# Kernel optimization log

Hardware: AMD Instinct MI355X
Metric: run time of the kernel (lower is better)

## Reference

```python
import jax, jax.numpy as jnp
import numpy as np

D_MODEL = 768
N_HEADS = 12
D_K = D_MODEL // N_HEADS
NEG = -1e9


def setup_inputs() -> dict:
    key = jax.random.key(0)
    ks = jax.random.split(key, 10)
    B, S = 2, 2048
    x = jax.random.normal(ks[0], (B, S, D_MODEL), dtype=jnp.float32)
    # causal mask, broadcastable over batch and heads
    mask = jnp.tril(jnp.ones((S, S), dtype=jnp.int32))[None, None]
    scale = 1.0 / np.sqrt(D_MODEL)
    def lin(k):
        return jax.random.normal(k, (D_MODEL, D_MODEL), dtype=jnp.float32) * scale
    return {
        "x": x, "mask": mask,
        "wq": lin(ks[1]), "bq": jnp.zeros((D_MODEL,), jnp.float32),
        "wk": lin(ks[2]), "bk": jnp.zeros((D_MODEL,), jnp.float32),
        "wv": lin(ks[3]), "bv": jnp.zeros((D_MODEL,), jnp.float32),
        "wo": lin(ks[4]), "bo": jnp.zeros((D_MODEL,), jnp.float32),
    }


def reference(x, mask, wq, bq, wk, bk, wv, bv, wo, bo):
    B, S, _ = x.shape
    def split_heads(t):  # [B,S,D] -> [B,H,S,dk]
        return t.reshape(B, S, N_HEADS, D_K).transpose(0, 2, 1, 3)
    q = split_heads(x @ wq + bq)
    k = split_heads(x @ wk + bk)
    v = split_heads(x @ wv + bv)
    scores = jnp.einsum("bhqd,bhkd->bhqk", q, k) / jnp.sqrt(jnp.float32(D_K))
    scores = jnp.where(mask == 0, NEG, scores)
    attn = jax.nn.softmax(scores, axis=-1)
    # dropout is identity in eval mode
    ctx = jnp.einsum("bhqk,bhkd->bhqd", attn, v)
    ctx = ctx.transpose(0, 2, 1, 3).reshape(B, S, D_MODEL)
    return ctx @ wo + bo
```

## Files before the change

kernel.cpp:

```cpp
#include <hip/hip_runtime.h>
#include <hip/hip_bf16.h>
#include <stdint.h>

#define DM   768
#define NH   12
#define DKH  64
#define BB   2
#define SS   2048
#define MT   (BB*SS)
#define NQKV (3*DM)

typedef __attribute__((ext_vector_type(8))) short short8;
typedef __attribute__((ext_vector_type(4))) float f32x4;

__device__ __forceinline__ unsigned short f2bf(float f) {
    union { float f; unsigned u; } v; v.f = f;
    unsigned r = v.u + 0x7fffu + ((v.u >> 16) & 1u);
    return (unsigned short)(r >> 16);
}

__device__ __forceinline__ void gload_lds16(const unsigned short* g, unsigned short* l) {
    __builtin_amdgcn_global_load_lds((const __attribute__((address_space(1))) void*)g,
                                     (__attribute__((address_space(3))) void*)l, 16, 0, 0);
}

__launch_bounds__(256)
__global__ void k_conv(const float* __restrict__ x, unsigned short* __restrict__ xb,
                       const float* __restrict__ wq, const float* __restrict__ wk,
                       const float* __restrict__ wv, const float* __restrict__ wo,
                       unsigned short* __restrict__ wT) {
    __shared__ float tile[32][33];
    const int t = threadIdx.x;
    if (blockIdx.x < 3072) {
        int i = blockIdx.x * 256 + t;
        const float4 v = ((const float4*)x)[i];
        ushort4 o;
        o.x = f2bf(v.x); o.y = f2bf(v.y); o.z = f2bf(v.z); o.w = f2bf(v.w);
        ((ushort4*)xb)[i] = o;
    } else {
        const int cid = blockIdx.x - 3072;
        const int sel = cid / 576;
        const int rem = cid - sel * 576;
        const int kb = rem / 24, nb = rem - (rem / 24) * 24;
        const float* w = (sel == 0) ? wq : (sel == 1) ? wk : (sel == 2) ? wv : wo;
        const int k0 = kb * 32, n0 = nb * 32;
        const int tx = t & 31, ty = t >> 5;
        #pragma unroll
        for (int j = 0; j < 4; j++)
            tile[ty + 8*j][tx] = w[(size_t)(k0 + ty + 8*j) * DM + n0 + tx];
        __syncthreads();
        #pragma unroll
        for (int j = 0; j < 4; j++)
            wT[(size_t)(sel*DM + n0 + ty + 8*j) * DM + k0 + tx] = f2bf(tile[tx][ty + 8*j]);
    }
}

__launch_bounds__(256, 4)
__global__ void k_gemm_qkv(const unsigned short* __restrict__ xb,
                           const unsigned short* __restrict__ wT,
                           const float* __restrict__ bq, const float* __restrict__ bk,
                           const float* __restrict__ bv,
                           unsigned short* __restrict__ Qb,
                           unsigned short* __restrict__ Kb,
                           unsigned short* __restrict__ Vt) {
    __shared__ __align__(16) unsigned short As[128*64];
    __shared__ __align__(16) unsigned short Bs[64*64];
    const int t = threadIdx.x;
    const int m0 = blockIdx.x * 128;
    const int n0 = blockIdx.y * 64;
    const int wid = t >> 6, lane = t & 63, q4 = lane >> 4, l16 = lane & 15;
    const int wm = (wid >> 1) * 64, wn = (wid & 1) * 32;

    const int srow = lane >> 3;
    const int scol = ((lane & 7) ^ srow) * 8;
    const unsigned short* Ag = xb + (size_t)(m0 + wid*8 + srow) * DM + scol;
    const unsigned short* Bg = wT + (size_t)(n0 + wid*8 + srow) * DM + scol;
    unsigned short* ldsA = &As[(wid*8)*64];
    unsigned short* ldsB = &Bs[(wid*8)*64];
    const int swz = (l16 & 7) * 8;

    f32x4 acc[4][2];
    for (int i = 0; i < 4; i++) for (int j = 0; j < 2; j++)
        acc[i][j] = (f32x4){0.f, 0.f, 0.f, 0.f};

    for (int kt = 0; kt < DM; kt += 64) {
        #pragma unroll
        for (int j = 0; j < 4; j++)
            gload_lds16(Ag + (size_t)(j*32) * DM + kt, ldsA + j*32*64);
        #pragma unroll
        for (int j = 0; j < 2; j++)
            gload_lds16(Bg + (size_t)(j*32) * DM + kt, ldsB + j*32*64);
        __syncthreads();
        #pragma unroll
        for (int kc = 0; kc < 2; kc++) {
            short8 af[4], bf[2];
            #pragma unroll
            for (int i = 0; i < 4; i++)
                af[i] = *(const short8*)&As[(wm + i*16 + l16)*64 + ((kc*32 + q4*8) ^ swz)];
            #pragma unroll
            for (int i = 0; i < 2; i++)
                bf[i] = *(const short8*)&Bs[(wn + i*16 + l16)*64 + ((kc*32 + q4*8) ^ swz)];
            #pragma unroll
            for (int mi = 0; mi < 4; mi++)
                #pragma unroll
                for (int ni = 0; ni < 2; ni++)
                    acc[mi][ni] = __builtin_amdgcn_mfma_f32_16x16x32_bf16(af[mi], bf[ni], acc[mi][ni], 0, 0, 0);
        }
        __syncthreads();
    }

    const int sel = n0 / DM;
    const float* bias = (sel == 0) ? bq : (sel == 1) ? bk : bv;
    for (int ni = 0; ni < 2; ni++) {
        const int col = n0 + wn + ni*16 + l16;
        const int c = col - sel * DM;
        const float bsv = bias[c];
        const int h = c >> 6, d = c & 63;
        for (int mi = 0; mi < 4; mi++) {
            for (int r = 0; r < 4; r++) {
                const int row = m0 + wm + mi*16 + q4*4 + r;
                const int b = row >> 11, s = row & 2047;
                const int bh = b * NH + h;
                float v = acc[mi][ni][r] + bsv;
                if (sel == 0) {
                    Qb[(bh*SS + s)*DKH + d] = f2bf(v * 0.125f);
                } else if (sel == 1) {
                    Kb[(bh*SS + s)*DKH + d] = f2bf(v);
                } else {
                    Vt[(bh*DKH + d)*SS + s] = f2bf(v);
                }
            }
        }
    }
}

__device__ const int UNITS[48] = {
  (15<<16)|(0<<8)|16, (31<<16)|(0<<8)|16, (31<<16)|(16<<8)|32, (30<<16)|(0<<8)|16,
  (14<<16)|(0<<8)|15, (29<<16)|(0<<8)|15, (29<<16)|(15<<8)|30, (28<<16)|(0<<8)|15, (30<<16)|(16<<8)|31,
  (13<<16)|(0<<8)|14, (27<<16)|(0<<8)|14, (27<<16)|(14<<8)|28, (26<<16)|(0<<8)|14, (28<<16)|(15<<8)|29,
  (12<<16)|(0<<8)|13, (25<<16)|(0<<8)|13, (25<<16)|(13<<8)|26, (24<<16)|(0<<8)|13, (26<<16)|(14<<8)|27,
  (11<<16)|(0<<8)|12, (23<<16)|(0<<8)|12, (23<<16)|(12<<8)|24, (22<<16)|(0<<8)|12, (24<<16)|(13<<8)|25,
  (10<<16)|(0<<8)|11, (21<<16)|(0<<8)|11, (21<<16)|(11<<8)|22, (20<<16)|(0<<8)|11, (22<<16)|(12<<8)|23,
  ( 9<<16)|(0<<8)|10, (19<<16)|(0<<8)|10, (19<<16)|(10<<8)|20, (18<<16)|(0<<8)|10, (20<<16)|(11<<8)|21,
  ( 8<<16)|(0<<8)| 9, (17<<16)|(0<<8)| 9, (17<<16)|( 9<<8)|18, (16<<16)|(0<<8)| 9, (18<<16)|(10<<8)|19,
  ( 7<<16)|(0<<8)| 8, (16<<16)|( 9<<8)|17,
  ( 6<<16)|(0<<8)| 7, ( 5<<16)|(0<<8)| 6, ( 4<<16)|(0<<8)| 5, ( 3<<16)|(0<<8)| 4,
  ( 2<<16)|(0<<8)| 3, ( 1<<16)|(0<<8)| 2, ( 0<<16)|(0<<8)| 1,
};

__launch_bounds__(256, 4)
__global__ void k_attn(const unsigned short* __restrict__ Qb,
                       const unsigned short* __restrict__ Kb,
                       const unsigned short* __restrict__ Vt,
                       unsigned short* __restrict__ ctx,
                       float* __restrict__ Opart, float* __restrict__ lpart) {
    __shared__ __align__(16) unsigned short Ks[2][64*64];
    __shared__ __align__(16) unsigned short Vs[2][64*64];
    __shared__ __align__(16) unsigned short P2[4][16*64];
    const int t = threadIdx.x;
    const int wid = t >> 6, lane = t & 63, q4 = lane >> 4, l16 = lane & 15;

    const int lin = blockIdx.x;
    const int bh = lin % 24;
    const int info = UNITS[lin / 24];
    const int qblk = info >> 16, t0 = (info >> 8) & 0xff, t1 = info & 0xff;
    const int b = bh / NH, h = bh - b * NH;
    const int qw = qblk * 64 + wid * 16;

    const unsigned short* Qp = Qb + (size_t)bh * SS * DKH;
    const unsigned short* Kp = Kb + (size_t)bh * SS * DKH;
    const unsigned short* Vp = Vt + (size_t)bh * DKH * SS;

    const int sr  = t >> 3;
    const int sc8 = (t & 7) * 8;
    const int scs = sc8 ^ ((sr & 7) * 8);
    const int swz = (l16 & 7) * 8;

    short8 qf[2];
    qf[0] = *(const short8*)(Qp + (size_t)(qw + l16)*DKH +      q4*8);
    qf[1] = *(const short8*)(Qp + (size_t)(qw + l16)*DKH + 32 + q4*8);

    f32x4 accO[4];
    #pragma unroll
    for (int j = 0; j < 4; j++) accO[j] = (f32x4){0.f, 0.f, 0.f, 0.f};
    float lacc = 0.f;

    {
        const int kb0 = t0 * 64;
        *(uint4*)&Ks[0][ sr    *64 + scs] = *(const uint4*)(Kp + (size_t)(kb0 + sr)     *DKH + sc8);
        *(uint4*)&Ks[0][(sr+32)*64 + scs] = *(const uint4*)(Kp + (size_t)(kb0 + sr + 32)*DKH + sc8);
        *(uint4*)&Vs[0][ sr    *64 + scs] = *(const uint4*)(Vp + (size_t) sr     *SS + kb0 + sc8);
        *(uint4*)&Vs[0][(sr+32)*64 + scs] = *(const uint4*)(Vp + (size_t)(sr+32) *SS + kb0 + sc8);
    }
    __syncthreads();

    for (int kt = t0; kt < t1; kt++) {
        const int cb = (kt - t0) & 1, nb = cb ^ 1;
        const bool hasN = (kt + 1 < t1);
        uint4 nk0, nk1, nv0, nv1;
        if (hasN) {
            const int kn = (kt + 1) * 64;
            nk0 = *(const uint4*)(Kp + (size_t)(kn + sr)      * DKH + sc8);
            nk1 = *(const uint4*)(Kp + (size_t)(kn + sr + 32) * DKH + sc8);
            nv0 = *(const uint4*)(Vp + (size_t)(sr)      * SS + kn + sc8);
            nv1 = *(const uint4*)(Vp + (size_t)(sr + 32) * SS + kn + sc8);
        }
        f32x4 St[4];
        #pragma unroll
        for (int ni = 0; ni < 4; ni++) St[ni] = (f32x4){0.f, 0.f, 0.f, 0.f};
        __builtin_amdgcn_s_setprio(1);
        #pragma unroll
        for (int ni = 0; ni < 4; ni++) {
            const int rbase = (ni*16 + l16) * 64;
            short8 kf0 = *(const short8*)&Ks[cb][rbase + ((     q4*8) ^ swz)];
            short8 kf1 = *(const short8*)&Ks[cb][rbase + ((32 + q4*8) ^ swz)];
            St[ni] = __builtin_amdgcn_mfma_f32_16x16x32_bf16(kf0, qf[0], St[ni], 0, 0, 0);
            St[ni] = __builtin_amdgcn_mfma_f32_16x16x32_bf16(kf1, qf[1], St[ni], 0, 0, 0);
        }
        __builtin_amdgcn_s_setprio(0);
        if (kt < qblk) {
            #pragma unroll
            for (int ni = 0; ni < 4; ni++) {
                float p0 = __expf(St[ni][0]), p1 = __expf(St[ni][1]);
                float p2 = __expf(St[ni][2]), p3 = __expf(St[ni][3]);
                lacc += (p0 + p1) + (p2 + p3);
                union { __hip_bfloat162 v; unsigned u; } u01, u23;
                u01.v = __float22bfloat162_rn(make_float2(p0, p1));
                u23.v = __float22bfloat162_rn(make_float2(p2, p3));
                uint2 pk; pk.x = u01.u; pk.y = u23.u;
                *(uint2*)&P2[wid][l16*64 + ((ni*16 + q4*4) ^ swz)] = pk;
            }
        } else {
            const int qrow = qw + l16;
            #pragma unroll
            for (int ni = 0; ni < 4; ni++) {
                const int key0 = kt*64 + ni*16 + q4*4;
                float p[4];
                #pragma unroll
                for (int r = 0; r < 4; r++) {
                    p[r] = (key0 + r > qrow) ? 0.f : __expf(St[ni][r]);
                    lacc += p[r];
                }
                union { __hip_bfloat162 v; unsigned u; } u01, u23;
                u01.v = __float22bfloat162_rn(make_float2(p[0], p[1]));
                u23.v = __float22bfloat162_rn(make_float2(p[2], p[3]));
                uint2 pk; pk.x = u01.u; pk.y = u23.u;
                *(uint2*)&P2[wid][l16*64 + ((ni*16 + q4*4) ^ swz)] = pk;
            }
        }
        asm volatile("s_waitcnt lgkmcnt(0)" ::: "memory");
        short8 pf[2];
        pf[0] = *(const short8*)&P2[wid][l16*64 + ((     q4*8) ^ swz)];
        pf[1] = *(const short8*)&P2[wid][l16*64 + ((32 + q4*8) ^ swz)];
        __builtin_amdgcn_s_setprio(1);
        #pragma unroll
        for (int ndi = 0; ndi < 4; ndi++) {
            const int rbase = (ndi*16 + l16) * 64;
            short8 vf0 = *(const short8*)&Vs[cb][rbase + ((     q4*8) ^ swz)];
            short8 vf1 = *(const short8*)&Vs[cb][rbase + ((32 + q4*8) ^ swz)];
            accO[ndi] = __builtin_amdgcn_mfma_f32_16x16x32_bf16(vf0, pf[0], accO[ndi], 0, 0, 0);
            accO[ndi] = __builtin_amdgcn_mfma_f32_16x16x32_bf16(vf1, pf[1], accO[ndi], 0, 0, 0);
        }
        __builtin_amdgcn_s_setprio(0);
        if (hasN) {
            *(uint4*)&Ks[nb][ sr    *64 + scs] = nk0;
            *(uint4*)&Ks[nb][(sr+32)*64 + scs] = nk1;
            *(uint4*)&Vs[nb][ sr    *64 + scs] = nv0;
            *(uint4*)&Vs[nb][(sr+32)*64 + scs] = nv1;
        }
        __syncthreads();
    }

    float l = lacc;
    l += __shfl_xor(l, 16);
    l += __shfl_xor(l, 32);

    if (qblk < 16) {
        const float inv = 1.0f / l;
        const size_t row = (size_t)(b*SS + qw + l16);
        #pragma unroll
        for (int ndi = 0; ndi < 4; ndi++) {
            ushort4 o;
            o.x = f2bf(accO[ndi][0] * inv);
            o.y = f2bf(accO[ndi][1] * inv);
            o.z = f2bf(accO[ndi][2] * inv);
            o.w = f2bf(accO[ndi][3] * inv);
            *(ushort4*)&ctx[row*DM + h*64 + ndi*16 + q4*4] = o;
        }
    } else {
        const int pair  = bh * 16 + (qblk - 16);
        const int chunk = (t0 != 0);
        const int qloc  = wid * 16 + l16;
        float* Op = Opart + ((size_t)pair * 2 + chunk) * 4096;
        #pragma unroll
        for (int ndi = 0; ndi < 4; ndi++)
            *(f32x4*)&Op[qloc*64 + ndi*16 + q4*4] = accO[ndi];
        if (q4 == 0) lpart[pair*128 + chunk*64 + qloc] = l;
    }
}

__launch_bounds__(256)
__global__ void k_combine(const float* __restrict__ Opart,
                          const float* __restrict__ lpart,
                          unsigned short* __restrict__ ctx) {
    const int pair = blockIdx.x;
    const int bh = pair >> 4, qblk = 16 + (pair & 15);
    const int b = bh / NH, h = bh - b * NH;
    const int t = threadIdx.x;
    const int q = t >> 2, dg = (t & 3) * 16;
    const float* P0 = Opart + (size_t)pair * 2 * 4096;
    const float* P1 = P0 + 4096;
    const float* L0 = lpart + pair * 128;
    const float inv = 1.0f / (L0[q] + L0[64 + q]);
    const size_t row = (size_t)(b*SS + qblk*64 + q);
    #pragma unroll
    for (int i = 0; i < 4; i++) {
        f32x4 a = *(const f32x4*)&P0[q*64 + dg + i*4];
        f32x4 c = *(const f32x4*)&P1[q*64 + dg + i*4];
        ushort4 o;
        o.x = f2bf((a[0] + c[0]) * inv);
        o.y = f2bf((a[1] + c[1]) * inv);
        o.z = f2bf((a[2] + c[2]) * inv);
        o.w = f2bf((a[3] + c[3]) * inv);
        *(ushort4*)&ctx[row*DM + h*64 + dg + i*4] = o;
    }
}

__launch_bounds__(256)
__global__ void k_gemm_proj(const unsigned short* __restrict__ ctx,
                            const unsigned short* __restrict__ woT,
                            const float* __restrict__ bo,
                            float* __restrict__ out) {
    __shared__ __align__(16) unsigned short As[128][32];
    __shared__ __align__(16) unsigned short Bs[64][32];
    const int t = threadIdx.x;
    const int m0 = blockIdx.x * 128;
    const int n0 = blockIdx.y * 64;
    const int wid = t >> 6, lane = t & 63, q4 = lane >> 4, l16 = lane & 15;
    const int wm = (wid >> 1) * 64, wn = (wid & 1) * 32;

    const int srowA = wid * 32 + (lane >> 2);
    const int srowB = wid * 16 + (lane >> 2);
    const int koff = (lane & 3) * 8;
    const unsigned short* AgL = ctx + (size_t)(m0 + srowA) * DM + koff;
    const unsigned short* AgH = AgL + (size_t)16 * DM;
    const unsigned short* BgL = woT + (size_t)(n0 + srowB) * DM + koff;
    unsigned short* ldsA1 = &As[wid*32][0];
    unsigned short* ldsA2 = &As[wid*32 + 16][0];
    unsigned short* ldsB1 = &Bs[wid*16][0];

    f32x4 acc[4][2];
    for (int i = 0; i < 4; i++) for (int j = 0; j < 2; j++)
        acc[i][j] = (f32x4){0.f, 0.f, 0.f, 0.f};

    for (int kt = 0; kt < DM; kt += 32) {
        gload_lds16(AgL + kt, ldsA1);
        gload_lds16(AgH + kt, ldsA2);
        gload_lds16(BgL + kt, ldsB1);
        __syncthreads();
        short8 af[4], bf[2];
        for (int i = 0; i < 4; i++) af[i] = *(const short8*)&As[wm + i*16 + l16][q4*8];
        for (int i = 0; i < 2; i++) bf[i] = *(const short8*)&Bs[wn + i*16 + l16][q4*8];
        for (int mi = 0; mi < 4; mi++)
            for (int ni = 0; ni < 2; ni++)
                acc[mi][ni] = __builtin_amdgcn_mfma_f32_16x16x32_bf16(af[mi], bf[ni], acc[mi][ni], 0, 0, 0);
        __syncthreads();
    }

    for (int ni = 0; ni < 2; ni++) {
        const int col = n0 + wn + ni*16 + l16;
        const float bsv = bo[col];
        for (int mi = 0; mi < 4; mi++) {
            for (int r = 0; r < 4; r++) {
                const int row = m0 + wm + mi*16 + q4*4 + r;
                out[(size_t)row * DM + col] = acc[mi][ni][r] + bsv;
            }
        }
    }
}

extern "C" void kernel_launch(void* const* d_in, const int* in_sizes, int n_in,
                              void* d_out, int out_size, void* d_ws, size_t ws_size,
                              hipStream_t stream) {
    const float* x  = (const float*)d_in[0];
    const float* wq = (const float*)d_in[2];
    const float* bq = (const float*)d_in[3];
    const float* wk = (const float*)d_in[4];
    const float* bk = (const float*)d_in[5];
    const float* wv = (const float*)d_in[6];
    const float* bv = (const float*)d_in[7];
    const float* wo = (const float*)d_in[8];
    const float* bo = (const float*)d_in[9];
    float* out = (float*)d_out;

    unsigned short* xb  = (unsigned short*)d_ws;
    unsigned short* wT  = xb + (size_t)MT * DM;
    unsigned short* Qb  = wT + (size_t)4 * DM * DM;
    unsigned short* Kb  = Qb + (size_t)BB * NH * SS * DKH;
    unsigned short* Vt  = Kb + (size_t)BB * NH * SS * DKH;
    unsigned short* ctx = Vt + (size_t)BB * NH * SS * DKH;
    float* Opart = (float*)(ctx + (size_t)MT * DM);
    float* lpart = Opart + (size_t)768 * 4096;

    k_conv<<<3072 + 2304, 256, 0, stream>>>(x, xb, wq, wk, wv, wo, wT);
    dim3 g1(MT / 128, NQKV / 64);
    k_gemm_qkv<<<g1, 256, 0, stream>>>(xb, wT, bq, bk, bv, Qb, Kb, Vt);
    k_attn<<<dim3(1152), 256, 0, stream>>>(Qb, Kb, Vt, ctx, Opart, lpart);
    k_combine<<<dim3(384), 256, 0, stream>>>(Opart, lpart, ctx);
    dim3 g3(MT / 128, DM / 64);
    k_gemm_proj<<<g3, 256, 0, stream>>>(ctx, wT + (size_t)3 * DM * DM, bo, out);
}
```

Before: 170.7 us.

## Stage V transpose through LDS and retile output projection to 64x64 swizzled tiles

In the QKV GEMM epilogue, V blocks now write their bf16 tile into shared memory with an XOR swizzle, then store transposed rows to Vt with 16-byte vector stores. The old path did strided 2-byte scattered stores. The output projection GEMM moves from 128x64 tiles with a K-step of 32 to 64x64 tiles with a K-step of 64 and swizzled LDS, doubling the grid and adding occupancy hints. This is meant to improve memory coalescing and occupancy, at the cost of an extra barrier in the epilogue and less reuse per tile in the projection.

```diff
diff --git a/kernel.cpp b/kernel.cpp
--- a/kernel.cpp
+++ b/kernel.cpp
@@ -110,26 +110,50 @@
     }
 
     const int sel = n0 / DM;
-    const float* bias = (sel == 0) ? bq : (sel == 1) ? bk : bv;
-    for (int ni = 0; ni < 2; ni++) {
-        const int col = n0 + wn + ni*16 + l16;
-        const int c = col - sel * DM;
-        const float bsv = bias[c];
-        const int h = c >> 6, d = c & 63;
-        for (int mi = 0; mi < 4; mi++) {
-            for (int r = 0; r < 4; r++) {
-                const int row = m0 + wm + mi*16 + q4*4 + r;
-                const int b = row >> 11, s = row & 2047;
-                const int bh = b * NH + h;
-                float v = acc[mi][ni][r] + bsv;
-                if (sel == 0) {
-                    Qb[(bh*SS + s)*DKH + d] = f2bf(v * 0.125f);
-                } else if (sel == 1) {
-                    Kb[(bh*SS + s)*DKH + d] = f2bf(v);
-                } else {
-                    Vt[(bh*DKH + d)*SS + s] = f2bf(v);
+    if (sel < 2) {
+        const float* bias = (sel == 0) ? bq : bk;
+        for (int ni = 0; ni < 2; ni++) {
+            const int col = n0 + wn + ni*16 + l16;
+            const int c = col - sel * DM;
+            const float bsv = bias[c];
+            const int h = c >> 6, d = c & 63;
+            for (int mi = 0; mi < 4; mi++) {
+                for (int r = 0; r < 4; r++) {
+                    const int row = m0 + wm + mi*16 + q4*4 + r;
+                    const int b = row >> 11, s = row & 2047;
+                    const int bh = b * NH + h;
+                    float v = acc[mi][ni][r] + bsv;
+                    if (sel == 0) Qb[(bh*SS + s)*DKH + d] = f2bf(v * 0.125f);
+                    else          Kb[(bh*SS + s)*DKH + d] = f2bf(v);
                 }
             }
+        }
+    } else {
+        const int h  = (n0 - 2*DM) >> 6;
+        const int bb = m0 >> 11, sbase = m0 & 2047;
+        const int bh = bb * NH + h;
+        #pragma unroll
+        for (int ni = 0; ni < 2; ni++) {
+            const int c = wn + ni*16 + l16;
+            const float bsv = bv[h*64 + c];
+            #pragma unroll
+            for (int mi = 0; mi < 4; mi++) {
+                const int rowb = wm + mi*16 + q4*4;
+                ushort4 o;
+                o.x = f2bf(acc[mi][ni][0] + bsv);
+                o.y = f2bf(acc[mi][ni][1] + bsv);
+                o.z = f2bf(acc[mi][ni][2] + bsv);
+                o.w = f2bf(acc[mi][ni][3] + bsv);
+                *(ushort4*)&As[c*128 + (rowb ^ ((c & 7) * 8))] = o;
+            }
+        }
+        __syncthreads();
+        const int d = t >> 2, sq = (t & 3) * 32;
+        unsigned short* Vg = Vt + ((size_t)bh*DKH + d)*SS + sbase + sq;
+        #pragma unroll
+        for (int j = 0; j < 4; j++) {
+            short8 v = *(const short8*)&As[d*128 + ((sq + j*8) ^ ((d & 7) * 8))];
+            *(short8*)&Vg[j*8] = v;
         }
     }
 }
@@ -326,51 +350,60 @@
     }
 }
 
-__launch_bounds__(256)
+__launch_bounds__(256, 4)
 __global__ void k_gemm_proj(const unsigned short* __restrict__ ctx,
                             const unsigned short* __restrict__ woT,
                             const float* __restrict__ bo,
                             float* __restrict__ out) {
-    __shared__ __align__(16) unsigned short As[128][32];
-    __shared__ __align__(16) unsigned short Bs[64][32];
+    __shared__ __align__(16) unsigned short As[64*64];
+    __shared__ __align__(16) unsigned short Bs[64*64];
     const int t = threadIdx.x;
-    const int m0 = blockIdx.x * 128;
+    const int m0 = blockIdx.x * 64;
     const int n0 = blockIdx.y * 64;
     const int wid = t >> 6, lane = t & 63, q4 = lane >> 4, l16 = lane & 15;
-    const int wm = (wid >> 1) * 64, wn = (wid & 1) * 32;
-
-    const int srowA = wid * 32 + (lane >> 2);
-    const int srowB = wid * 16 + (lane >> 2);
-    const int koff = (lane & 3) * 8;
-    const unsigned short* AgL = ctx + (size_t)(m0 + srowA) * DM + koff;
-    const unsigned short* AgH = AgL + (size_t)16 * DM;
-    const unsigned short* BgL = woT + (size_t)(n0 + srowB) * DM + koff;
-    unsigned short* ldsA1 = &As[wid*32][0];
-    unsigned short* ldsA2 = &As[wid*32 + 16][0];
-    unsigned short* ldsB1 = &Bs[wid*16][0];
-
-    f32x4 acc[4][2];
-    for (int i = 0; i < 4; i++) for (int j = 0; j < 2; j++)
+    const int wm = (wid >> 1) * 32, wn = (wid & 1) * 32;
+
+    const int srow = lane >> 3;
+    const int scol = ((lane & 7) ^ srow) * 8;
+    const unsigned short* Ag = ctx + (size_t)(m0 + wid*8 + srow) * DM + scol;
+    const unsigned short* Bg = woT + (size_t)(n0 + wid*8 + srow) * DM + scol;
+    unsigned short* ldsA = &As[(wid*8)*64];
+    unsigned short* ldsB = &Bs[(wid*8)*64];
+    const int swz = (l16 & 7) * 8;
+
+    f32x4 acc[2][2];
+    for (int i = 0; i < 2; i++) for (int j = 0; j < 2; j++)
         acc[i][j] = (f32x4){0.f, 0.f, 0.f, 0.f};
 
-    for (int kt = 0; kt < DM; kt += 32) {
-        gload_lds16(AgL + kt, ldsA1);
-        gload_lds16(AgH + kt, ldsA2);
-        gload_lds16(BgL + kt, ldsB1);
-        __syncthreads();
-        short8 af[4], bf[2];
-        for (int i = 0; i < 4; i++) af[i] = *(const short8*)&As[wm + i*16 + l16][q4*8];
-        for (int i = 0; i < 2; i++) bf[i] = *(const short8*)&Bs[wn + i*16 + l16][q4*8];
-        for (int mi = 0; mi < 4; mi++)
-            for (int ni = 0; ni < 2; ni++)
-                acc[mi][ni] = __builtin_amdgcn_mfma_f32_16x16x32_bf16(af[mi], bf[ni], acc[mi][ni], 0, 0, 0);
+    for (int kt = 0; kt < DM; kt += 64) {
+        #pragma unroll
+        for (int j = 0; j < 2; j++) {
+            gload_lds16(Ag + (size_t)(j*32) * DM + kt, ldsA + j*32*64);
+            gload_lds16(Bg + (size_t)(j*32) * DM + kt, ldsB + j*32*64);
+        }
+        __syncthreads();
+        #pragma unroll
+        for (int kc = 0; kc < 2; kc++) {
+            short8 af[2], bf[2];
+            #pragma unroll
+            for (int i = 0; i < 2; i++)
+                af[i] = *(const short8*)&As[(wm + i*16 + l16)*64 + ((kc*32 + q4*8) ^ swz)];
+            #pragma unroll
+            for (int i = 0; i < 2; i++)
+                bf[i] = *(const short8*)&Bs[(wn + i*16 + l16)*64 + ((kc*32 + q4*8) ^ swz)];
+            #pragma unroll
+            for (int mi = 0; mi < 2; mi++)
+                #pragma unroll
+                for (int ni = 0; ni < 2; ni++)
+                    acc[mi][ni] = __builtin_amdgcn_mfma_f32_16x16x32_bf16(af[mi], bf[ni], acc[mi][ni], 0, 0, 0);
+        }
         __syncthreads();
     }
 
     for (int ni = 0; ni < 2; ni++) {
         const int col = n0 + wn + ni*16 + l16;
         const float bsv = bo[col];
-        for (int mi = 0; mi < 4; mi++) {
+        for (int mi = 0; mi < 2; mi++) {
             for (int r = 0; r < 4; r++) {
                 const int row = m0 + wm + mi*16 + q4*4 + r;
                 out[(size_t)row * DM + col] = acc[mi][ni][r] + bsv;
@@ -407,6 +440,6 @@
     k_gemm_qkv<<<g1, 256, 0, stream>>>(xb, wT, bq, bk, bv, Qb, Kb, Vt);
     k_attn<<<dim3(1152), 256, 0, stream>>>(Qb, Kb, Vt, ctx, Opart, lpart);
     k_combine<<<dim3(384), 256, 0, stream>>>(Opart, lpart, ctx);
-    dim3 g3(MT / 128, DM / 64);
+    dim3 g3(MT / 64, DM / 64);
     k_gemm_proj<<<g3, 256, 0, stream>>>(ctx, wT + (size_t)3 * DM * DM, bo, out);
 }
```

Result: faster. 159.0 us (-6.9%).
